# Kernel optimization log

Measured on AMD Instinct MI355X. Metric: run time of the kernel, lower is better.

Reference implementation:

```python
import jax, jax.numpy as jnp
import numpy as np

B, L, DIN, H, E, K = 64, 256, 768, 64, 8, 2
S = 16  # sqrt(L): token<->feature grid side
LOSS_COEF = 1e-2


def gelu(x):
    return jax.nn.gelu(x, approximate=False)  # torch nn.GELU (exact erf)


def cv_squared(v):
    v = v.astype(jnp.float32)
    return jnp.var(v, ddof=1) / (jnp.mean(v) ** 2 + 1e-10)


def setup_inputs() -> dict:
    key = jax.random.key(0)
    ks = jax.random.split(key, 16)
    rn = lambda k, shape, s=0.02: jax.random.normal(k, shape, jnp.float32) * s
    lap = jnp.array([[0., 1., 0.], [1., -4., 1.], [0., 1., 0.]], jnp.float32)
    return {
        "x": jax.random.normal(ks[0], (B, L, DIN), jnp.float32),
        "dte": jax.random.normal(ks[1], (B, L, DIN), jnp.float32),
        "w_gate": rn(ks[2], (L, E), 1.0),
        "W_exp": rn(ks[3], (E, DIN, H)), "b_exp": jnp.zeros((E, H), jnp.float32),
        "W_sh": rn(ks[4], (DIN, H)), "b_sh": jnp.zeros((H,), jnp.float32),
        "ln_g": jnp.ones((H,), jnp.float32), "ln_b": jnp.zeros((H,), jnp.float32),
        "W_px": rn(ks[5], (H, 2 * H)), "b_px": jnp.zeros((2 * H,), jnp.float32),
        "conv_sh": jnp.tile(lap[None, None], (H, 1, 1, 1)),  # depthwise Laplacian [H,1,3,3]
        "W_pxx": rn(ks[6], (H, H)), "b_pxx": jnp.zeros((H,), jnp.float32),
        "W_dte": rn(ks[7], (H, H)), "b_dte": jnp.zeros((H,), jnp.float32),
        "W_dteall": rn(ks[8], (H, H)), "b_dteall": jnp.zeros((H,), jnp.float32),
        "W_rgb": rn(ks[9], (DIN, H)), "b_rgb": jnp.zeros((H,), jnp.float32),
        "W_fx": rn(ks[10], (H, H)), "b_fx": jnp.zeros((H,), jnp.float32),
        "W_fmod": rn(ks[11], (H, H)), "b_fmod": jnp.zeros((H,), jnp.float32),
        "W_fxx": rn(ks[12], (H, H)), "b_fxx": jnp.zeros((H,), jnp.float32),
    }


def reference(x, dte, w_gate, W_exp, b_exp, W_sh, b_sh, ln_g, ln_b, W_px, b_px,
              conv_sh, W_pxx, b_pxx, W_dte, b_dte, W_dteall, b_dteall,
              W_rgb, b_rgb, W_fx, b_fx, W_fmod, b_fmod, W_fxx, b_fxx):
    # ---- top-k gating (clean logits; noisy_gating=False / eval) ----
    logits = dte.mean(-1) @ w_gate                     # [B,E]
    topv, topi = jax.lax.top_k(logits, K)
    topg = jax.nn.softmax(topv, axis=1)
    gates = jnp.zeros_like(logits).at[jnp.arange(B)[:, None], topi].set(topg)
    importance = gates.sum(0)
    load = (gates > 0).sum(0).astype(jnp.float32)
    loss = LOSS_COEF * (cv_squared(importance) + cv_squared(load))
    # ---- sparse dispatch / expert Linear / weighted combine (dense-equivalent) ----
    y = jnp.einsum('be,bld,edh->blh', gates, dte, W_exp) + (gates @ b_exp)[:, None, :]
    # ---- shared expert Linear + Shared block ----
    sh = dte @ W_sh + b_sh                             # [B,L,H]
    shortcut = sh
    t = (sh - sh.mean(-1, keepdims=True)) * jax.lax.rsqrt(sh.var(-1, keepdims=True) + 1e-6)
    t = t * ln_g + ln_b
    t = t @ W_px + b_px                                # [B,L,2H]
    t1, t2 = t[..., :H], t[..., H:]
    f = t1.transpose(0, 2, 1).reshape(B, H, S, S)      # token2feature
    f = jax.lax.conv_general_dilated(f, conv_sh, (1, 1), 'SAME', feature_group_count=H)
    t1 = f.reshape(B, H, L).transpose(0, 2, 1)         # feature2token
    sh = (gelu(t1) * t2) @ W_pxx + b_pxx + shortcut
    # ---- combine MoE and shared streams ----
    dte_tok = (y @ W_dte + b_dte) + (sh @ W_dteall + b_dteall)
    rgb_tok = x @ W_rgb + b_rgb
    # ---- Fusion (its self.norm was overwritten to GELU; token<->feature round-trip is identity) ----
    shortcut = rgb_tok
    a = gelu(rgb_tok) @ W_fx + b_fx
    m = gelu(dte_tok) @ W_fmod + b_fmod
    out = (gelu(m) * a) @ W_fxx + b_fxx + shortcut     # [B,L,H]
    return out, loss
```

## Files before the change

kernel.cpp:

```cpp
#include <hip/hip_runtime.h>
#include <hip/hip_bf16.h>
#include <math.h>

typedef unsigned short u16;
typedef unsigned int u32;
typedef __attribute__((ext_vector_type(8))) short bf16x8;
typedef __attribute__((ext_vector_type(4))) float f32x4;


__device__ __forceinline__ float bf2f(u16 u) {
    union { u32 i; float f; } x; x.i = ((u32)u) << 16; return x.f;
}
__device__ __forceinline__ u16 f2bf(float f) {
    union { __hip_bfloat16 h; u16 u; } x;
    x.h = __float2bfloat16(f);
    return x.u;
}
__device__ __forceinline__ u32 pack2(float a, float b) {
    union { __hip_bfloat162 h; u32 u; } x;
    x.h = __float22bfloat162_rn(make_float2(a, b));
    return x.u;
}
__device__ __forceinline__ float wsum(float v) {
    #pragma unroll
    for (int o = 1; o < 64; o <<= 1) v += __shfl_xor(v, o, 64);
    return v;
}
__device__ __forceinline__ float gelu_f(float x) {
    return 0.5f * x * (1.0f + erff(x * 0.70710678118654752440f));
}

__global__ __launch_bounds__(256) void k_gate_part(const float* __restrict__ dte,
                                                   const float* __restrict__ w_gate,
                                                   float* __restrict__ partial) {
    __shared__ float dmeanS[64];
    int p = blockIdx.x, tid = threadIdx.x, w = tid >> 6, lane = tid & 63;
    #pragma unroll
    for (int h = 0; h < 2; h++) {
        float4 v[8][3];
        #pragma unroll
        for (int i = 0; i < 8; i++) {
            const float* pr = dte + ((size_t)p * 64 + w * 16 + h * 8 + i) * 768;
            #pragma unroll
            for (int j = 0; j < 3; j++)
                v[i][j] = *(const float4*)(pr + (lane + j * 64) * 4);
        }
        #pragma unroll
        for (int i = 0; i < 8; i++) {
            float s = 0.f;
            #pragma unroll
            for (int j = 0; j < 3; j++)
                s += v[i][j].x + v[i][j].y + v[i][j].z + v[i][j].w;
            s = wsum(s);
            if (lane == 0) dmeanS[w * 16 + h * 8 + i] = s * (1.f / 768.f);
        }
    }
    __syncthreads();
    if (w == 0) {
        float dm = dmeanS[lane];
        int wl = (p & 3) * 64 + lane;
        #pragma unroll
        for (int e = 0; e < 8; e++) {
            float s = wsum(dm * w_gate[wl * 8 + e]);
            if (lane == 0) partial[p * 8 + e] = s;
        }
    }
}

__global__ __launch_bounds__(256) void k_gate_fin(const float* __restrict__ partial,
                                                  const float* __restrict__ b_exp,
                                                  int* __restrict__ topi,
                                                  float* __restrict__ topg,
                                                  float* __restrict__ bias_y,
                                                  float* __restrict__ loss_out) {
    __shared__ float gS[64 * 8];
    __shared__ int i0S[64], i1S[64];
    __shared__ float g0S[64], g1S[64];
    int tid = threadIdx.x;
    if (tid < 64) {
        float lg[8];
        #pragma unroll
        for (int e = 0; e < 8; e++)
            lg[e] = partial[(tid * 4 + 0) * 8 + e] + partial[(tid * 4 + 1) * 8 + e] +
                    partial[(tid * 4 + 2) * 8 + e] + partial[(tid * 4 + 3) * 8 + e];
        int i0 = 0; float v0 = lg[0];
        #pragma unroll
        for (int e = 1; e < 8; e++) if (lg[e] > v0) { v0 = lg[e]; i0 = e; }
        int i1 = -1; float v1 = -1e30f;
        #pragma unroll
        for (int e = 0; e < 8; e++) if (e != i0 && lg[e] > v1) { v1 = lg[e]; i1 = e; }
        if (i1 < 0) i1 = (i0 + 1) & 7;
        float e2 = expf(v1 - v0);
        float g0 = 1.f / (1.f + e2);
        float g1 = e2 / (1.f + e2);
        #pragma unroll
        for (int e = 0; e < 8; e++) gS[tid * 8 + e] = 0.f;
        gS[tid * 8 + i0] = g0;
        gS[tid * 8 + i1] = g1;
        i0S[tid] = i0; i1S[tid] = i1; g0S[tid] = g0; g1S[tid] = g1;
        topi[tid * 2] = i0; topi[tid * 2 + 1] = i1;
        topg[tid * 2] = g0; topg[tid * 2 + 1] = g1;
    }
    __syncthreads();
    for (int idx = tid; idx < 4096; idx += 256) {
        int b = idx >> 6, h = idx & 63;
        bias_y[idx] = g0S[b] * b_exp[i0S[b] * 64 + h] + g1S[b] * b_exp[i1S[b] * 64 + h];
    }
    if (tid < 64) {
        float g[8];
        #pragma unroll
        for (int e = 0; e < 8; e++) g[e] = gS[tid * 8 + e];
        float imp[8], ld[8];
        #pragma unroll
        for (int e = 0; e < 8; e++) {
            imp[e] = wsum(g[e]);
            ld[e]  = wsum(g[e] > 0.f ? 1.f : 0.f);
        }
        if (tid == 0) {
            float l = 0.f;
            {
                float s = 0.f;
                #pragma unroll
                for (int e = 0; e < 8; e++) s += imp[e];
                float mn = s / 8.f, v = 0.f;
                #pragma unroll
                for (int e = 0; e < 8; e++) { float d = imp[e] - mn; v += d * d; }
                l += (v / 7.f) / (mn * mn + 1e-10f);
            }
            {
                float s = 0.f;
                #pragma unroll
                for (int e = 0; e < 8; e++) s += ld[e];
                float mn = s / 8.f, v = 0.f;
                #pragma unroll
                for (int e = 0; e < 8; e++) { float d = ld[e] - mn; v += d * d; }
                l += (v / 7.f) / (mn * mn + 1e-10f);
            }
            loss_out[0] = 0.01f * l;
        }
    }
}

__global__ __launch_bounds__(256) void k_gemm3(const float* __restrict__ dte,
                                               const float* __restrict__ x,
                                               const float* __restrict__ W_sh,
                                               const float* __restrict__ b_sh,
                                               const float* __restrict__ W_exp,
                                               const int* __restrict__ topi,
                                               const float* __restrict__ topg,
                                               const float* __restrict__ bias_y,
                                               const float* __restrict__ W_rgb,
                                               const float* __restrict__ b_rgb,
                                               float* __restrict__ buf_sh,
                                               u16* __restrict__ buf_y,
                                               float* __restrict__ out_rgb) {
    __shared__ __align__(16) u16 As[64 * 72];
    __shared__ __align__(16) u16 Wt0[64 * 72];
    __shared__ __align__(16) u16 Wt1[64 * 72];
    int bid = blockIdx.x;
    bool fused = bid < 256;
    int row0 = fused ? bid * 64 : (bid - 256) * 64;
    int b = row0 >> 8;
    int tid = threadIdx.x, wv = tid >> 6, lane = tid & 63;
    int m = lane & 15, quad = lane >> 4;

    const float* A  = fused ? dte : x;
    const float* Wb = fused ? W_sh : W_rgb;
    const float* We0 = W_exp;
    const float* We1 = W_exp;
    float g0 = 0.f, g1 = 0.f;
    if (fused) {
        We0 = W_exp + (size_t)topi[2 * b] * 49152;
        We1 = W_exp + (size_t)topi[2 * b + 1] * 49152;
        g0 = topg[2 * b]; g1 = topg[2 * b + 1];
    }

    float4 pa[2][2];
    float  pw0[16];
    float  pw1[16];
    const int a_r  = tid >> 3;
    const int a_k8 = (tid & 7) * 8;
    const int w_n  = tid & 63;
    const int w_k0 = (tid >> 6) * 16;

    auto loadA = [&](int kc) {
        #pragma unroll
        for (int j = 0; j < 2; j++) {
            const float* src = A + (size_t)(row0 + a_r + j * 32) * 768 + kc * 64 + a_k8;
            pa[j][0] = *(const float4*)(src);
            pa[j][1] = *(const float4*)(src + 4);
        }
    };
    auto loadW = [&](int kc) {
        #pragma unroll
        for (int j = 0; j < 16; j++)
            pw0[j] = Wb[(size_t)(kc * 64 + w_k0 + j) * 64 + w_n];
        if (fused) {
            #pragma unroll
            for (int j = 0; j < 16; j++) {
                size_t off = (size_t)(kc * 64 + w_k0 + j) * 64 + w_n;
                pw1[j] = g0 * We0[off] + g1 * We1[off];
            }
        }
    };
    auto stageLDS = [&]() {
        #pragma unroll
        for (int j = 0; j < 2; j++) {
            uint4 d;
            d.x = pack2(pa[j][0].x, pa[j][0].y);
            d.y = pack2(pa[j][0].z, pa[j][0].w);
            d.z = pack2(pa[j][1].x, pa[j][1].y);
            d.w = pack2(pa[j][1].z, pa[j][1].w);
            *(uint4*)&As[(a_r + j * 32) * 72 + a_k8] = d;
        }
        {
            uint4 d0, d1;
            d0.x = pack2(pw0[0],  pw0[1]);  d0.y = pack2(pw0[2],  pw0[3]);
            d0.z = pack2(pw0[4],  pw0[5]);  d0.w = pack2(pw0[6],  pw0[7]);
            d1.x = pack2(pw0[8],  pw0[9]);  d1.y = pack2(pw0[10], pw0[11]);
            d1.z = pack2(pw0[12], pw0[13]); d1.w = pack2(pw0[14], pw0[15]);
            *(uint4*)&Wt0[w_n * 72 + w_k0]     = d0;
            *(uint4*)&Wt0[w_n * 72 + w_k0 + 8] = d1;
        }
        if (fused) {
            uint4 d0, d1;
            d0.x = pack2(pw1[0],  pw1[1]);  d0.y = pack2(pw1[2],  pw1[3]);
            d0.z = pack2(pw1[4],  pw1[5]);  d0.w = pack2(pw1[6],  pw1[7]);
            d1.x = pack2(pw1[8],  pw1[9]);  d1.y = pack2(pw1[10], pw1[11]);
            d1.z = pack2(pw1[12], pw1[13]); d1.w = pack2(pw1[14], pw1[15]);
            *(uint4*)&Wt1[w_n * 72 + w_k0]     = d0;
            *(uint4*)&Wt1[w_n * 72 + w_k0 + 8] = d1;
        }
    };

    f32x4 z = {0.f, 0.f, 0.f, 0.f};
    f32x4 s0 = z, s1 = z, s2 = z, s3 = z;
    f32x4 y0 = z, y1 = z, y2 = z, y3 = z;

    loadA(0); loadW(0);
    for (int kc = 0; kc < 12; kc++) {
        __syncthreads();
        stageLDS();
        __syncthreads();
        if (kc < 11) { loadA(kc + 1); loadW(kc + 1); }
        const int ar = (wv * 16 + m) * 72;
        bf16x8 a0 = *(const bf16x8*)&As[ar + quad * 8];
        bf16x8 a1 = *(const bf16x8*)&As[ar + 32 + quad * 8];
        #pragma unroll
        for (int t = 0; t < 4; t++) {
            const int br = (t * 16 + m) * 72;
            bf16x8 b0 = *(const bf16x8*)&Wt0[br + quad * 8];
            bf16x8 b1 = *(const bf16x8*)&Wt0[br + 32 + quad * 8];
            f32x4* sp = (t == 0) ? &s0 : (t == 1) ? &s1 : (t == 2) ? &s2 : &s3;
            *sp = __builtin_amdgcn_mfma_f32_16x16x32_bf16(a0, b0, *sp, 0, 0, 0);
            *sp = __builtin_amdgcn_mfma_f32_16x16x32_bf16(a1, b1, *sp, 0, 0, 0);
            if (fused) {
                bf16x8 c0 = *(const bf16x8*)&Wt1[br + quad * 8];
                bf16x8 c1 = *(const bf16x8*)&Wt1[br + 32 + quad * 8];
                f32x4* yp = (t == 0) ? &y0 : (t == 1) ? &y1 : (t == 2) ? &y2 : &y3;
                *yp = __builtin_amdgcn_mfma_f32_16x16x32_bf16(a0, c0, *yp, 0, 0, 0);
                *yp = __builtin_amdgcn_mfma_f32_16x16x32_bf16(a1, c1, *yp, 0, 0, 0);
            }
        }
    }

    f32x4 accs0[4] = {s0, s1, s2, s3};
    f32x4 accs1[4] = {y0, y1, y2, y3};
    #pragma unroll
    for (int t = 0; t < 4; t++) {
        int col = t * 16 + m;
        if (fused) {
            float bs = b_sh[col];
            float by = bias_y[b * 64 + col];
            #pragma unroll
            for (int i = 0; i < 4; i++) {
                int r = row0 + wv * 16 + quad * 4 + i;
                buf_sh[(size_t)r * 64 + col] = accs0[t][i] + bs;
                buf_y[(size_t)r * 64 + col]  = f2bf(accs1[t][i] + by);
            }
        } else {
            float br = b_rgb[col];
            #pragma unroll
            for (int i = 0; i < 4; i++) {
                int r = row0 + wv * 16 + quad * 4 + i;
                out_rgb[(size_t)r * 64 + col] = accs0[t][i] + br;
            }
        }
    }
}

__global__ __launch_bounds__(256) void k_lnpx(const float* __restrict__ buf_sh,
                                              const float* __restrict__ ln_g,
                                              const float* __restrict__ ln_b,
                                              const float* __restrict__ W_px,
                                              const float* __restrict__ b_px,
                                              u16* __restrict__ t1, u16* __restrict__ t2) {
    __shared__ __align__(16) float T[32 * 68];
    __shared__ __align__(16) float Wpx[8192];
    int r0 = blockIdx.x * 32;
    int tid = threadIdx.x, w = tid >> 6, lane = tid & 63;
    #pragma unroll
    for (int j = 0; j < 8; j++) {
        const float* g = W_px + (size_t)(w * 64 + j * 256) * 4 + lane * 4;
        float* l = Wpx + (w * 64 + j * 256) * 4;
        __builtin_amdgcn_global_load_lds(
            (const __attribute__((address_space(1))) unsigned int*)g,
            (__attribute__((address_space(3))) unsigned int*)l,
            16, 0, 0);
    }
    float lnG = ln_g[lane], lnB = ln_b[lane];
    for (int i = 0; i < 8; i++) {
        int l = w * 8 + i;
        float v = buf_sh[(size_t)(r0 + l) * 64 + lane];
        float mean = wsum(v) * (1.f / 64.f);
        float d = v - mean;
        float var = wsum(d * d) * (1.f / 64.f);
        T[l * 68 + lane] = d * rsqrtf(var + 1e-6f) * lnG + lnB;
    }
    __syncthreads();
    int rg = tid >> 4, cg = tid & 15;
    float acc1[2][4] = {}, acc2[2][4] = {};
    const float* tr = T + rg * 2 * 68;
    #pragma unroll 2
    for (int k4 = 0; k4 < 64; k4 += 4) {
        float4 av0 = *(const float4*)(tr + k4);
        float4 av1 = *(const float4*)(tr + 68 + k4);
        const float a0s[4] = {av0.x, av0.y, av0.z, av0.w};
        const float a1s[4] = {av1.x, av1.y, av1.z, av1.w};
        #pragma unroll
        for (int q = 0; q < 4; q++) {
            int kk = k4 + q;
            float a0 = a0s[q], a1 = a1s[q];
            float4 w1 = *(const float4*)(Wpx + kk * 128 + cg * 4);
            float4 w2 = *(const float4*)(Wpx + kk * 128 + 64 + cg * 4);
            acc1[0][0] += a0 * w1.x; acc1[0][1] += a0 * w1.y; acc1[0][2] += a0 * w1.z; acc1[0][3] += a0 * w1.w;
            acc1[1][0] += a1 * w1.x; acc1[1][1] += a1 * w1.y; acc1[1][2] += a1 * w1.z; acc1[1][3] += a1 * w1.w;
            acc2[0][0] += a0 * w2.x; acc2[0][1] += a0 * w2.y; acc2[0][2] += a0 * w2.z; acc2[0][3] += a0 * w2.w;
            acc2[1][0] += a1 * w2.x; acc2[1][1] += a1 * w2.y; acc2[1][2] += a1 * w2.z; acc2[1][3] += a1 * w2.w;
        }
    }
    float4 b1 = *(const float4*)(b_px + cg * 4);
    float4 b2 = *(const float4*)(b_px + 64 + cg * 4);
    #pragma unroll
    for (int i = 0; i < 2; i++) {
        int r = r0 + rg * 2 + i;
        u32* d1 = (u32*)(t1 + (size_t)r * 64 + cg * 4);
        d1[0] = pack2(acc1[i][0] + b1.x, acc1[i][1] + b1.y);
        d1[1] = pack2(acc1[i][2] + b1.z, acc1[i][3] + b1.w);
        u32* d2 = (u32*)(t2 + (size_t)r * 64 + cg * 4);
        d2[0] = pack2(acc2[i][0] + b2.x, acc2[i][1] + b2.y);
        d2[1] = pack2(acc2[i][2] + b2.z, acc2[i][3] + b2.w);
    }
}

__global__ __launch_bounds__(256) void k_tail(const u16* __restrict__ t1,
                                              const u16* __restrict__ t2,
                                              const float* __restrict__ conv_sh,
                                              const float* __restrict__ W_pxx,
                                              const float* __restrict__ b_pxx,
                                              const float* __restrict__ buf_sh,
                                              const u16* __restrict__ buf_y,
                                              const float* __restrict__ W_dte,
                                              const float* __restrict__ b_dte,
                                              const float* __restrict__ W_dteall,
                                              const float* __restrict__ b_dteall,
                                              const float* __restrict__ W_fx,
                                              const float* __restrict__ b_fx,
                                              const float* __restrict__ W_fmod,
                                              const float* __restrict__ b_fmod,
                                              const float* __restrict__ W_fxx,
                                              const float* __restrict__ b_fxx,
                                              float* __restrict__ out) {
    __shared__ __align__(16) float C0[32 * 68];
    __shared__ __align__(16) float GA[32 * 68];
    __shared__ __align__(16) float SH1[32 * 68];
    __shared__ __align__(16) float GM[32 * 68];
    __shared__ __align__(16) u16   Ybh[32 * 72];
    __shared__ __align__(16) float WL[2][4096];
    int r0 = blockIdx.x * 32;
    int tid = threadIdx.x, w = tid >> 6, lane = tid & 63;
    int rg = tid >> 4, cg = tid & 15;

    auto stage_w = [&](const float* __restrict__ Wsrc, int half) {
        const float* g = Wsrc + w * 1024 + lane * 4;
        float* l = &WL[half][w * 1024];
        #pragma unroll
        for (int j = 0; j < 4; j++) {
            __builtin_amdgcn_global_load_lds(
                (const __attribute__((address_space(1))) unsigned int*)(g + j * 256),
                (__attribute__((address_space(3))) unsigned int*)(l + j * 256),
                16, 0, 0);
        }
    };

    stage_w(W_pxx, 0);

    stage_w(W_dte, 1);
    float4 rsv[2];
    #pragma unroll
    for (int i = 0; i < 2; i++) {
        int r = rg * 2 + i;
        uint2 v = *(const uint2*)(buf_y + (size_t)(r0 + r) * 64 + cg * 4);
        *(uint2*)(&Ybh[r * 72 + cg * 4]) = v;
        rsv[i] = *(const float4*)(out + (size_t)(r0 + r) * 64 + cg * 4);
        GA[r * 68 + cg * 4 + 0] = gelu_f(rsv[i].x);
        GA[r * 68 + cg * 4 + 1] = gelu_f(rsv[i].y);
        GA[r * 68 + cg * 4 + 2] = gelu_f(rsv[i].z);
        GA[r * 68 + cg * 4 + 3] = gelu_f(rsv[i].w);
    }
    {
        float c0 = conv_sh[lane * 9 + 0], c1 = conv_sh[lane * 9 + 1], c2 = conv_sh[lane * 9 + 2];
        float c3 = conv_sh[lane * 9 + 3], c4 = conv_sh[lane * 9 + 4], c5 = conv_sh[lane * 9 + 5];
        float c6 = conv_sh[lane * 9 + 6], c7 = conv_sh[lane * 9 + 7], c8 = conv_sh[lane * 9 + 8];
        #pragma unroll
        for (int i = 0; i < 8; i++) {
            int l = w * 8 + i;
            int gr = r0 + l;
            int pix = gr & 255, ii = pix >> 4, jj = pix & 15;
            const u16* p = t1 + (size_t)gr * 64 + lane;
            float c = c4 * bf2f(p[0]);
            if (ii > 0) {
                c += c1 * bf2f(p[-1024]);
                if (jj > 0)  c += c0 * bf2f(p[-1024 - 64]);
                if (jj < 15) c += c2 * bf2f(p[-1024 + 64]);
            }
            if (jj > 0)  c += c3 * bf2f(p[-64]);
            if (jj < 15) c += c5 * bf2f(p[64]);
            if (ii < 15) {
                c += c7 * bf2f(p[1024]);
                if (jj > 0)  c += c6 * bf2f(p[1024 - 64]);
                if (jj < 15) c += c8 * bf2f(p[1024 + 64]);
            }
            C0[l * 68 + lane] = gelu_f(c) * bf2f(t2[(size_t)gr * 64 + lane]);
        }
    }
    __syncthreads();

    {
        float acc[2][4] = {};
        const float* ur = C0 + rg * 2 * 68;
        #pragma unroll 4
        for (int k4 = 0; k4 < 64; k4 += 4) {
            float4 av0 = *(const float4*)(ur + k4);
            float4 av1 = *(const float4*)(ur + 68 + k4);
            const float a0s[4] = {av0.x, av0.y, av0.z, av0.w};
            const float a1s[4] = {av1.x, av1.y, av1.z, av1.w};
            #pragma unroll
            for (int q = 0; q < 4; q++) {
                float a0 = a0s[q], a1 = a1s[q];
                float4 wv = *(const float4*)(&WL[0][(k4 + q) * 64 + cg * 4]);
                acc[0][0] += a0 * wv.x; acc[0][1] += a0 * wv.y; acc[0][2] += a0 * wv.z; acc[0][3] += a0 * wv.w;
                acc[1][0] += a1 * wv.x; acc[1][1] += a1 * wv.y; acc[1][2] += a1 * wv.z; acc[1][3] += a1 * wv.w;
            }
        }
        float4 bp = *(const float4*)(b_pxx + cg * 4);
        #pragma unroll
        for (int i = 0; i < 2; i++) {
            int r = rg * 2 + i;
            float4 shv = *(const float4*)(buf_sh + (size_t)(r0 + r) * 64 + cg * 4);
            *(float4*)(SH1 + r * 68 + cg * 4) =
                make_float4(acc[i][0] + bp.x + shv.x, acc[i][1] + bp.y + shv.y,
                            acc[i][2] + bp.z + shv.z, acc[i][3] + bp.w + shv.w);
        }
    }
    __syncthreads();

    float accC[2][4] = {};
    stage_w(W_dteall, 0);
    {
        const u16* yr = Ybh + rg * 2 * 72;
        #pragma unroll 4
        for (int k4 = 0; k4 < 64; k4 += 4) {
            uint2 yv0 = *(const uint2*)(yr + k4);
            uint2 yv1 = *(const uint2*)(yr + 72 + k4);
            const float y0s[4] = {bf2f((u16)(yv0.x & 0xffffu)), bf2f((u16)(yv0.x >> 16)),
                                  bf2f((u16)(yv0.y & 0xffffu)), bf2f((u16)(yv0.y >> 16))};
            const float y1s[4] = {bf2f((u16)(yv1.x & 0xffffu)), bf2f((u16)(yv1.x >> 16)),
                                  bf2f((u16)(yv1.y & 0xffffu)), bf2f((u16)(yv1.y >> 16))};
            #pragma unroll
            for (int q = 0; q < 4; q++) {
                float y0 = y0s[q], y1 = y1s[q];
                float4 wv = *(const float4*)(&WL[1][(k4 + q) * 64 + cg * 4]);
                accC[0][0] += y0 * wv.x; accC[0][1] += y0 * wv.y; accC[0][2] += y0 * wv.z; accC[0][3] += y0 * wv.w;
                accC[1][0] += y1 * wv.x; accC[1][1] += y1 * wv.y; accC[1][2] += y1 * wv.z; accC[1][3] += y1 * wv.w;
            }
        }
    }
    __syncthreads();

    stage_w(W_fx, 1);
    {
        const float* sr = SH1 + rg * 2 * 68;
        #pragma unroll 4
        for (int k4 = 0; k4 < 64; k4 += 4) {
            float4 av0 = *(const float4*)(sr + k4);
            float4 av1 = *(const float4*)(sr + 68 + k4);
            const float s0s[4] = {av0.x, av0.y, av0.z, av0.w};
            const float s1s[4] = {av1.x, av1.y, av1.z, av1.w};
            #pragma unroll
            for (int q = 0; q < 4; q++) {
                float s0 = s0s[q], s1 = s1s[q];
                float4 wv = *(const float4*)(&WL[0][(k4 + q) * 64 + cg * 4]);
                accC[0][0] += s0 * wv.x; accC[0][1] += s0 * wv.y; accC[0][2] += s0 * wv.z; accC[0][3] += s0 * wv.w;
                accC[1][0] += s1 * wv.x; accC[1][1] += s1 * wv.y; accC[1][2] += s1 * wv.z; accC[1][3] += s1 * wv.w;
            }
        }
        float4 bd1 = *(const float4*)(b_dte + cg * 4);
        float4 bd2 = *(const float4*)(b_dteall + cg * 4);
        #pragma unroll
        for (int i = 0; i < 2; i++) {
            int r = rg * 2 + i;
            *(float4*)(GM + r * 68 + cg * 4) =
                make_float4(gelu_f(accC[i][0] + bd1.x + bd2.x), gelu_f(accC[i][1] + bd1.y + bd2.y),
                            gelu_f(accC[i][2] + bd1.z + bd2.z), gelu_f(accC[i][3] + bd1.w + bd2.w));
        }
    }
    __syncthreads();

    float accA[2][4] = {};
    stage_w(W_fmod, 0);
    {
        const float* ga = GA + rg * 2 * 68;
        #pragma unroll 4
        for (int k4 = 0; k4 < 64; k4 += 4) {
            float4 av0 = *(const float4*)(ga + k4);
            float4 av1 = *(const float4*)(ga + 68 + k4);
            const float a0s[4] = {av0.x, av0.y, av0.z, av0.w};
            const float a1s[4] = {av1.x, av1.y, av1.z, av1.w};
            #pragma unroll
            for (int q = 0; q < 4; q++) {
                float a0 = a0s[q], a1 = a1s[q];
                float4 wv = *(const float4*)(&WL[1][(k4 + q) * 64 + cg * 4]);
                accA[0][0] += a0 * wv.x; accA[0][1] += a0 * wv.y; accA[0][2] += a0 * wv.z; accA[0][3] += a0 * wv.w;
                accA[1][0] += a1 * wv.x; accA[1][1] += a1 * wv.y; accA[1][2] += a1 * wv.z; accA[1][3] += a1 * wv.w;
            }
        }
    }
    __syncthreads();

    stage_w(W_fxx, 1);
    {
        float accM[2][4] = {};
        const float* gm = GM + rg * 2 * 68;
        #pragma unroll 4
        for (int k4 = 0; k4 < 64; k4 += 4) {
            float4 av0 = *(const float4*)(gm + k4);
            float4 av1 = *(const float4*)(gm + 68 + k4);
            const float m0s[4] = {av0.x, av0.y, av0.z, av0.w};
            const float m1s[4] = {av1.x, av1.y, av1.z, av1.w};
            #pragma unroll
            for (int q = 0; q < 4; q++) {
                float m0 = m0s[q], m1 = m1s[q];
                float4 wv = *(const float4*)(&WL[0][(k4 + q) * 64 + cg * 4]);
                accM[0][0] += m0 * wv.x; accM[0][1] += m0 * wv.y; accM[0][2] += m0 * wv.z; accM[0][3] += m0 * wv.w;
                accM[1][0] += m1 * wv.x; accM[1][1] += m1 * wv.y; accM[1][2] += m1 * wv.z; accM[1][3] += m1 * wv.w;
            }
        }
        float4 bx = *(const float4*)(b_fx + cg * 4);
        float4 bm = *(const float4*)(b_fmod + cg * 4);
        #pragma unroll
        for (int i = 0; i < 2; i++) {
            int r = rg * 2 + i;
            float a0 = accA[i][0] + bx.x, a1 = accA[i][1] + bx.y, a2 = accA[i][2] + bx.z, a3 = accA[i][3] + bx.w;
            float m0 = accM[i][0] + bm.x, m1 = accM[i][1] + bm.y, m2 = accM[i][2] + bm.z, m3 = accM[i][3] + bm.w;
            *(float4*)(C0 + r * 68 + cg * 4) =
                make_float4(gelu_f(m0) * a0, gelu_f(m1) * a1, gelu_f(m2) * a2, gelu_f(m3) * a3);
        }
    }
    __syncthreads();

    {
        float acc[2][4] = {};
        const float* pr = C0 + rg * 2 * 68;
        #pragma unroll 4
        for (int k4 = 0; k4 < 64; k4 += 4) {
            float4 av0 = *(const float4*)(pr + k4);
            float4 av1 = *(const float4*)(pr + 68 + k4);
            const float p0s[4] = {av0.x, av0.y, av0.z, av0.w};
            const float p1s[4] = {av1.x, av1.y, av1.z, av1.w};
            #pragma unroll
            for (int q = 0; q < 4; q++) {
                float p0 = p0s[q], p1 = p1s[q];
                float4 wv = *(const float4*)(&WL[1][(k4 + q) * 64 + cg * 4]);
                acc[0][0] += p0 * wv.x; acc[0][1] += p0 * wv.y; acc[0][2] += p0 * wv.z; acc[0][3] += p0 * wv.w;
                acc[1][0] += p1 * wv.x; acc[1][1] += p1 * wv.y; acc[1][2] += p1 * wv.z; acc[1][3] += p1 * wv.w;
            }
        }
        float4 bo = *(const float4*)(b_fxx + cg * 4);
        #pragma unroll
        for (int i = 0; i < 2; i++) {
            int r = rg * 2 + i;
            *(float4*)(out + (size_t)(r0 + r) * 64 + cg * 4) =
                make_float4(acc[i][0] + bo.x + rsv[i].x, acc[i][1] + bo.y + rsv[i].y,
                            acc[i][2] + bo.z + rsv[i].z, acc[i][3] + bo.w + rsv[i].w);
        }
    }
}

extern "C" void kernel_launch(void* const* d_in, const int* in_sizes, int n_in,
                              void* d_out, int out_size, void* d_ws, size_t ws_size,
                              hipStream_t stream) {
    const float* x       = (const float*)d_in[0];
    const float* dte     = (const float*)d_in[1];
    const float* w_gate  = (const float*)d_in[2];
    const float* W_exp   = (const float*)d_in[3];
    const float* b_exp   = (const float*)d_in[4];
    const float* W_sh    = (const float*)d_in[5];
    const float* b_sh    = (const float*)d_in[6];
    const float* ln_g    = (const float*)d_in[7];
    const float* ln_b    = (const float*)d_in[8];
    const float* W_px    = (const float*)d_in[9];
    const float* b_px    = (const float*)d_in[10];
    const float* conv_sh = (const float*)d_in[11];
    const float* W_pxx   = (const float*)d_in[12];
    const float* b_pxx   = (const float*)d_in[13];
    const float* W_dte   = (const float*)d_in[14];
    const float* b_dte   = (const float*)d_in[15];
    const float* W_dteall= (const float*)d_in[16];
    const float* b_dteall= (const float*)d_in[17];
    const float* W_rgb   = (const float*)d_in[18];
    const float* b_rgb   = (const float*)d_in[19];
    const float* W_fx    = (const float*)d_in[20];
    const float* b_fx    = (const float*)d_in[21];
    const float* W_fmod  = (const float*)d_in[22];
    const float* b_fmod  = (const float*)d_in[23];
    const float* W_fxx   = (const float*)d_in[24];
    const float* b_fxx   = (const float*)d_in[25];

    float* out = (float*)d_out;

    float* wsf    = (float*)d_ws;
    float* partial= wsf;
    int*   topi   = (int*)(wsf + 2048);
    float* topg   = wsf + 2176;
    float* bias_y = wsf + 2304;
    float* buf_sh = wsf + 8192;
    u16*   buf_y  = (u16*)(wsf + 8192 + 1048576);
    u16*   t1     = (u16*)(wsf + 8192 + 1048576 + 524288);
    u16*   t2     = (u16*)(wsf + 8192 + 1048576 + 524288*2);

    hipLaunchKernelGGL(k_gate_part, dim3(256), dim3(256), 0, stream, dte, w_gate, partial);
    hipLaunchKernelGGL(k_gate_fin, dim3(1), dim3(256), 0, stream,
                       partial, b_exp, topi, topg, bias_y, out + 1048576);
    hipLaunchKernelGGL(k_gemm3, dim3(512), dim3(256), 0, stream,
                       dte, x, W_sh, b_sh, W_exp, topi, topg, bias_y, W_rgb, b_rgb,
                       buf_sh, buf_y, out);
    hipLaunchKernelGGL(k_lnpx, dim3(512), dim3(256), 0, stream,
                       buf_sh, ln_g, ln_b, W_px, b_px, t1, t2);
    hipLaunchKernelGGL(k_tail, dim3(512), dim3(256), 0, stream,
                       t1, t2, conv_sh, W_pxx, b_pxx, buf_sh, buf_y,
                       W_dte, b_dte, W_dteall, b_dteall,
                       W_fx, b_fx, W_fmod, b_fmod, W_fxx, b_fxx, out);

    (void)in_sizes; (void)n_in; (void)out_size; (void)ws_size;
}
```

Before: 237.6 us.

## Merge gating finalize into MoE GEMM and overlap rgb GEMM with gate reduction

Removes the single-block gate finalize kernel. Each MoE GEMM block now recomputes its own batch's top-2 selection and softmax from the partial logits, and block 0 also computes the load-balancing loss. The rgb projection GEMM moves into the same launch as the gate partial reduction, so those independent tasks share one grid. This cuts one launch and one serial single-block stage, at the cost of redundant top-k work in every MoE block and less balanced block types in the first kernel.

Result: slower. 251.7 us (+5.9%).

```diff
diff --git a/kernel.cpp b/kernel.cpp
--- a/kernel.cpp
+++ b/kernel.cpp
@@ -30,86 +30,189 @@
     return 0.5f * x * (1.0f + erff(x * 0.70710678118654752440f));
 }
 
-__global__ __launch_bounds__(256) void k_gate_part(const float* __restrict__ dte,
-                                                   const float* __restrict__ w_gate,
-                                                   float* __restrict__ partial) {
+__global__ __launch_bounds__(256) void k_front(const float* __restrict__ dte,
+                                               const float* __restrict__ w_gate,
+                                               float* __restrict__ partial,
+                                               const float* __restrict__ x,
+                                               const float* __restrict__ W_rgb,
+                                               const float* __restrict__ b_rgb,
+                                               float* __restrict__ out_rgb) {
     __shared__ float dmeanS[64];
-    int p = blockIdx.x, tid = threadIdx.x, w = tid >> 6, lane = tid & 63;
-    #pragma unroll
-    for (int h = 0; h < 2; h++) {
-        float4 v[8][3];
-        #pragma unroll
-        for (int i = 0; i < 8; i++) {
-            const float* pr = dte + ((size_t)p * 64 + w * 16 + h * 8 + i) * 768;
-            #pragma unroll
-            for (int j = 0; j < 3; j++)
-                v[i][j] = *(const float4*)(pr + (lane + j * 64) * 4);
-        }
-        #pragma unroll
-        for (int i = 0; i < 8; i++) {
-            float s = 0.f;
-            #pragma unroll
-            for (int j = 0; j < 3; j++)
-                s += v[i][j].x + v[i][j].y + v[i][j].z + v[i][j].w;
-            s = wsum(s);
-            if (lane == 0) dmeanS[w * 16 + h * 8 + i] = s * (1.f / 768.f);
-        }
-    }
-    __syncthreads();
-    if (w == 0) {
-        float dm = dmeanS[lane];
-        int wl = (p & 3) * 64 + lane;
-        #pragma unroll
-        for (int e = 0; e < 8; e++) {
-            float s = wsum(dm * w_gate[wl * 8 + e]);
-            if (lane == 0) partial[p * 8 + e] = s;
-        }
-    }
-}
-
-__global__ __launch_bounds__(256) void k_gate_fin(const float* __restrict__ partial,
-                                                  const float* __restrict__ b_exp,
-                                                  int* __restrict__ topi,
-                                                  float* __restrict__ topg,
-                                                  float* __restrict__ bias_y,
-                                                  float* __restrict__ loss_out) {
-    __shared__ float gS[64 * 8];
-    __shared__ int i0S[64], i1S[64];
-    __shared__ float g0S[64], g1S[64];
-    int tid = threadIdx.x;
-    if (tid < 64) {
-        float lg[8];
+    __shared__ __align__(16) u16 As[64 * 72];
+    __shared__ __align__(16) u16 Wt0[64 * 72];
+    int bid = blockIdx.x;
+    int tid = threadIdx.x, w = tid >> 6, lane = tid & 63;
+
+    if (bid < 256) {
+        int p = bid;
+        #pragma unroll
+        for (int h = 0; h < 2; h++) {
+            float4 v[8][3];
+            #pragma unroll
+            for (int i = 0; i < 8; i++) {
+                const float* pr = dte + ((size_t)p * 64 + w * 16 + h * 8 + i) * 768;
+                #pragma unroll
+                for (int j = 0; j < 3; j++)
+                    v[i][j] = *(const float4*)(pr + (lane + j * 64) * 4);
+            }
+            #pragma unroll
+            for (int i = 0; i < 8; i++) {
+                float s = 0.f;
+                #pragma unroll
+                for (int j = 0; j < 3; j++)
+                    s += v[i][j].x + v[i][j].y + v[i][j].z + v[i][j].w;
+                s = wsum(s);
+                if (lane == 0) dmeanS[w * 16 + h * 8 + i] = s * (1.f / 768.f);
+            }
+        }
+        __syncthreads();
+        if (w == 0) {
+            float dm = dmeanS[lane];
+            int wl = (p & 3) * 64 + lane;
+            #pragma unroll
+            for (int e = 0; e < 8; e++) {
+                float s = wsum(dm * w_gate[wl * 8 + e]);
+                if (lane == 0) partial[p * 8 + e] = s;
+            }
+        }
+        return;
+    }
+
+    int row0 = (bid - 256) * 64;
+    int m = lane & 15, quad = lane >> 4;
+
+    float4 pa[2][2];
+    float  pw0[16];
+    const int a_r  = tid >> 3;
+    const int a_k8 = (tid & 7) * 8;
+    const int w_n  = tid & 63;
+    const int w_k0 = (tid >> 6) * 16;
+
+    auto loadA = [&](int kc) {
+        #pragma unroll
+        for (int j = 0; j < 2; j++) {
+            const float* src = x + (size_t)(row0 + a_r + j * 32) * 768 + kc * 64 + a_k8;
+            pa[j][0] = *(const float4*)(src);
+            pa[j][1] = *(const float4*)(src + 4);
+        }
+    };
+    auto loadW = [&](int kc) {
+        #pragma unroll
+        for (int j = 0; j < 16; j++)
+            pw0[j] = W_rgb[(size_t)(kc * 64 + w_k0 + j) * 64 + w_n];
+    };
+    auto stageLDS = [&]() {
+        #pragma unroll
+        for (int j = 0; j < 2; j++) {
+            uint4 d;
+            d.x = pack2(pa[j][0].x, pa[j][0].y);
+            d.y = pack2(pa[j][0].z, pa[j][0].w);
+            d.z = pack2(pa[j][1].x, pa[j][1].y);
+            d.w = pack2(pa[j][1].z, pa[j][1].w);
+            *(uint4*)&As[(a_r + j * 32) * 72 + a_k8] = d;
+        }
+        uint4 d0, d1;
+        d0.x = pack2(pw0[0],  pw0[1]);  d0.y = pack2(pw0[2],  pw0[3]);
+        d0.z = pack2(pw0[4],  pw0[5]);  d0.w = pack2(pw0[6],  pw0[7]);
+        d1.x = pack2(pw0[8],  pw0[9]);  d1.y = pack2(pw0[10], pw0[11]);
+        d1.z = pack2(pw0[12], pw0[13]); d1.w = pack2(pw0[14], pw0[15]);
+        *(uint4*)&Wt0[w_n * 72 + w_k0]     = d0;
+        *(uint4*)&Wt0[w_n * 72 + w_k0 + 8] = d1;
+    };
+
+    f32x4 z = {0.f, 0.f, 0.f, 0.f};
+    f32x4 s0 = z, s1 = z, s2 = z, s3 = z;
+
+    loadA(0); loadW(0);
+    for (int kc = 0; kc < 12; kc++) {
+        __syncthreads();
+        stageLDS();
+        __syncthreads();
+        if (kc < 11) { loadA(kc + 1); loadW(kc + 1); }
+        const int ar = ((tid >> 6) * 16 + m) * 72;
+        bf16x8 a0 = *(const bf16x8*)&As[ar + quad * 8];
+        bf16x8 a1 = *(const bf16x8*)&As[ar + 32 + quad * 8];
+        #pragma unroll
+        for (int t = 0; t < 4; t++) {
+            const int br = (t * 16 + m) * 72;
+            bf16x8 b0 = *(const bf16x8*)&Wt0[br + quad * 8];
+            bf16x8 b1 = *(const bf16x8*)&Wt0[br + 32 + quad * 8];
+            f32x4* sp = (t == 0) ? &s0 : (t == 1) ? &s1 : (t == 2) ? &s2 : &s3;
+            *sp = __builtin_amdgcn_mfma_f32_16x16x32_bf16(a0, b0, *sp, 0, 0, 0);
+            *sp = __builtin_amdgcn_mfma_f32_16x16x32_bf16(a1, b1, *sp, 0, 0, 0);
+        }
+    }
+
+    f32x4 accs0[4] = {s0, s1, s2, s3};
+    #pragma unroll
+    for (int t = 0; t < 4; t++) {
+        int col = t * 16 + m;
+        float br = b_rgb[col];
+        #pragma unroll
+        for (int i = 0; i < 4; i++) {
+            int r = row0 + (tid >> 6) * 16 + quad * 4 + i;
+            out_rgb[(size_t)r * 64 + col] = accs0[t][i] + br;
+        }
+    }
+}
+
+__global__ __launch_bounds__(256) void k_moe(const float* __restrict__ dte,
+                                             const float* __restrict__ W_sh,
+                                             const float* __restrict__ b_sh,
+                                             const float* __restrict__ W_exp,
+                                             const float* __restrict__ b_exp,
+                                             const float* __restrict__ partial,
+                                             float* __restrict__ buf_sh,
+                                             u16* __restrict__ buf_y,
+                                             float* __restrict__ loss_out) {
+    __shared__ __align__(16) u16 As[64 * 72];
+    __shared__ __align__(16) u16 Wt0[64 * 72];
+    __shared__ __align__(16) u16 Wt1[64 * 72];
+    int bid = blockIdx.x;
+    int row0 = bid * 64;
+    int b = bid >> 2;
+    int tid = threadIdx.x, wv = tid >> 6, lane = tid & 63;
+    int m = lane & 15, quad = lane >> 4;
+
+    float lg[8];
+    #pragma unroll
+    for (int e = 0; e < 8; e++)
+        lg[e] = partial[(b * 4 + 0) * 8 + e] + partial[(b * 4 + 1) * 8 + e] +
+                partial[(b * 4 + 2) * 8 + e] + partial[(b * 4 + 3) * 8 + e];
+    int i0 = 0; float v0 = lg[0];
+    #pragma unroll
+    for (int e = 1; e < 8; e++) if (lg[e] > v0) { v0 = lg[e]; i0 = e; }
+    int i1 = -1; float v1 = -1e30f;
+    #pragma unroll
+    for (int e = 0; e < 8; e++) if (e != i0 && lg[e] > v1) { v1 = lg[e]; i1 = e; }
+    if (i1 < 0) i1 = (i0 + 1) & 7;
+    float e2 = expf(v1 - v0);
+    float g0 = 1.f / (1.f + e2);
+    float g1 = e2 / (1.f + e2);
+    const float* We0 = W_exp + (size_t)i0 * 49152;
+    const float* We1 = W_exp + (size_t)i1 * 49152;
+
+    if (bid == 0 && tid < 64) {
+        float lgl[8];
         #pragma unroll
         for (int e = 0; e < 8; e++)
-            lg[e] = partial[(tid * 4 + 0) * 8 + e] + partial[(tid * 4 + 1) * 8 + e] +
-                    partial[(tid * 4 + 2) * 8 + e] + partial[(tid * 4 + 3) * 8 + e];
-        int i0 = 0; float v0 = lg[0];
-        #pragma unroll
-        for (int e = 1; e < 8; e++) if (lg[e] > v0) { v0 = lg[e]; i0 = e; }
-        int i1 = -1; float v1 = -1e30f;
-        #pragma unroll
-        for (int e = 0; e < 8; e++) if (e != i0 && lg[e] > v1) { v1 = lg[e]; i1 = e; }
-        if (i1 < 0) i1 = (i0 + 1) & 7;
-        float e2 = expf(v1 - v0);
-        float g0 = 1.f / (1.f + e2);
-        float g1 = e2 / (1.f + e2);
-        #pragma unroll
-        for (int e = 0; e < 8; e++) gS[tid * 8 + e] = 0.f;
-        gS[tid * 8 + i0] = g0;
-        gS[tid * 8 + i1] = g1;
-        i0S[tid] = i0; i1S[tid] = i1; g0S[tid] = g0; g1S[tid] = g1;
-        topi[tid * 2] = i0; topi[tid * 2 + 1] = i1;
-        topg[tid * 2] = g0; topg[tid * 2 + 1] = g1;
-    }
-    __syncthreads();
-    for (int idx = tid; idx < 4096; idx += 256) {
-        int b = idx >> 6, h = idx & 63;
-        bias_y[idx] = g0S[b] * b_exp[i0S[b] * 64 + h] + g1S[b] * b_exp[i1S[b] * 64 + h];
-    }
-    if (tid < 64) {
+            lgl[e] = partial[(tid * 4 + 0) * 8 + e] + partial[(tid * 4 + 1) * 8 + e] +
+                     partial[(tid * 4 + 2) * 8 + e] + partial[(tid * 4 + 3) * 8 + e];
+        int li0 = 0; float lv0 = lgl[0];
+        #pragma unroll
+        for (int e = 1; e < 8; e++) if (lgl[e] > lv0) { lv0 = lgl[e]; li0 = e; }
+        int li1 = -1; float lv1 = -1e30f;
+        #pragma unroll
+        for (int e = 0; e < 8; e++) if (e != li0 && lgl[e] > lv1) { lv1 = lgl[e]; li1 = e; }
+        if (li1 < 0) li1 = (li0 + 1) & 7;
+        float le2 = expf(lv1 - lv0);
+        float lg0 = 1.f / (1.f + le2);
+        float lg1 = le2 / (1.f + le2);
         float g[8];
         #pragma unroll
-        for (int e = 0; e < 8; e++) g[e] = gS[tid * 8 + e];
+        for (int e = 0; e < 8; e++) g[e] = 0.f;
+        g[li0] = lg0;
+        g[li1] = lg1;
         float imp[8], ld[8];
         #pragma unroll
         for (int e = 0; e < 8; e++) {
@@ -139,41 +242,6 @@
             loss_out[0] = 0.01f * l;
         }
     }
-}
-
-__global__ __launch_bounds__(256) void k_gemm3(const float* __restrict__ dte,
-                                               const float* __restrict__ x,
-                                               const float* __restrict__ W_sh,
-                                               const float* __restrict__ b_sh,
-                                               const float* __restrict__ W_exp,
-                                               const int* __restrict__ topi,
-                                               const float* __restrict__ topg,
-                                               const float* __restrict__ bias_y,
-                                               const float* __restrict__ W_rgb,
-                                               const float* __restrict__ b_rgb,
-                                               float* __restrict__ buf_sh,
-                                               u16* __restrict__ buf_y,
-                                               float* __restrict__ out_rgb) {
-    __shared__ __align__(16) u16 As[64 * 72];
-    __shared__ __align__(16) u16 Wt0[64 * 72];
-    __shared__ __align__(16) u16 Wt1[64 * 72];
-    int bid = blockIdx.x;
-    bool fused = bid < 256;
-    int row0 = fused ? bid * 64 : (bid - 256) * 64;
-    int b = row0 >> 8;
-    int tid = threadIdx.x, wv = tid >> 6, lane = tid & 63;
-    int m = lane & 15, quad = lane >> 4;
-
-    const float* A  = fused ? dte : x;
-    const float* Wb = fused ? W_sh : W_rgb;
-    const float* We0 = W_exp;
-    const float* We1 = W_exp;
-    float g0 = 0.f, g1 = 0.f;
-    if (fused) {
-        We0 = W_exp + (size_t)topi[2 * b] * 49152;
-        We1 = W_exp + (size_t)topi[2 * b + 1] * 49152;
-        g0 = topg[2 * b]; g1 = topg[2 * b + 1];
-    }
 
     float4 pa[2][2];
     float  pw0[16];
@@ -186,7 +254,7 @@
     auto loadA = [&](int kc) {
         #pragma unroll
         for (int j = 0; j < 2; j++) {
-            const float* src = A + (size_t)(row0 + a_r + j * 32) * 768 + kc * 64 + a_k8;
+            const float* src = dte + (size_t)(row0 + a_r + j * 32) * 768 + kc * 64 + a_k8;
             pa[j][0] = *(const float4*)(src);
             pa[j][1] = *(const float4*)(src + 4);
         }
@@ -194,13 +262,11 @@
     auto loadW = [&](int kc) {
         #pragma unroll
         for (int j = 0; j < 16; j++)
-            pw0[j] = Wb[(size_t)(kc * 64 + w_k0 + j) * 64 + w_n];
-        if (fused) {
-            #pragma unroll
-            for (int j = 0; j < 16; j++) {
-                size_t off = (size_t)(kc * 64 + w_k0 + j) * 64 + w_n;
-                pw1[j] = g0 * We0[off] + g1 * We1[off];
-            }
+            pw0[j] = W_sh[(size_t)(kc * 64 + w_k0 + j) * 64 + w_n];
+        #pragma unroll
+        for (int j = 0; j < 16; j++) {
+            size_t off = (size_t)(kc * 64 + w_k0 + j) * 64 + w_n;
+            pw1[j] = g0 * We0[off] + g1 * We1[off];
         }
     };
     auto stageLDS = [&]() {
@@ -222,7 +288,7 @@
             *(uint4*)&Wt0[w_n * 72 + w_k0]     = d0;
             *(uint4*)&Wt0[w_n * 72 + w_k0 + 8] = d1;
         }
-        if (fused) {
+        {
             uint4 d0, d1;
             d0.x = pack2(pw1[0],  pw1[1]);  d0.y = pack2(pw1[2],  pw1[3]);
             d0.z = pack2(pw1[4],  pw1[5]);  d0.w = pack2(pw1[6],  pw1[7]);
@@ -254,13 +320,11 @@
             f32x4* sp = (t == 0) ? &s0 : (t == 1) ? &s1 : (t == 2) ? &s2 : &s3;
             *sp = __builtin_amdgcn_mfma_f32_16x16x32_bf16(a0, b0, *sp, 0, 0, 0);
             *sp = __builtin_amdgcn_mfma_f32_16x16x32_bf16(a1, b1, *sp, 0, 0, 0);
-            if (fused) {
-                bf16x8 c0 = *(const bf16x8*)&Wt1[br + quad * 8];
-                bf16x8 c1 = *(const bf16x8*)&Wt1[br + 32 + quad * 8];
-                f32x4* yp = (t == 0) ? &y0 : (t == 1) ? &y1 : (t == 2) ? &y2 : &y3;
-                *yp = __builtin_amdgcn_mfma_f32_16x16x32_bf16(a0, c0, *yp, 0, 0, 0);
-                *yp = __builtin_amdgcn_mfma_f32_16x16x32_bf16(a1, c1, *yp, 0, 0, 0);
-            }
+            bf16x8 c0 = *(const bf16x8*)&Wt1[br + quad * 8];
+            bf16x8 c1 = *(const bf16x8*)&Wt1[br + 32 + quad * 8];
+            f32x4* yp = (t == 0) ? &y0 : (t == 1) ? &y1 : (t == 2) ? &y2 : &y3;
+            *yp = __builtin_amdgcn_mfma_f32_16x16x32_bf16(a0, c0, *yp, 0, 0, 0);
+            *yp = __builtin_amdgcn_mfma_f32_16x16x32_bf16(a1, c1, *yp, 0, 0, 0);
         }
     }
 
@@ -269,22 +333,13 @@
     #pragma unroll
     for (int t = 0; t < 4; t++) {
         int col = t * 16 + m;
-        if (fused) {
-            float bs = b_sh[col];
-            float by = bias_y[b * 64 + col];
-            #pragma unroll
-            for (int i = 0; i < 4; i++) {
-                int r = row0 + wv * 16 + quad * 4 + i;
-                buf_sh[(size_t)r * 64 + col] = accs0[t][i] + bs;
-                buf_y[(size_t)r * 64 + col]  = f2bf(accs1[t][i] + by);
-            }
-        } else {
-            float br = b_rgb[col];
-            #pragma unroll
-            for (int i = 0; i < 4; i++) {
-                int r = row0 + wv * 16 + quad * 4 + i;
-                out_rgb[(size_t)r * 64 + col] = accs0[t][i] + br;
-            }
+        float bs = b_sh[col];
+        float by = g0 * b_exp[i0 * 64 + col] + g1 * b_exp[i1 * 64 + col];
+        #pragma unroll
+        for (int i = 0; i < 4; i++) {
+            int r = row0 + wv * 16 + quad * 4 + i;
+            buf_sh[(size_t)r * 64 + col] = accs0[t][i] + bs;
+            buf_y[(size_t)r * 64 + col]  = f2bf(accs1[t][i] + by);
         }
     }
 }
@@ -631,20 +686,16 @@
 
     float* wsf    = (float*)d_ws;
     float* partial= wsf;
-    int*   topi   = (int*)(wsf + 2048);
-    float* topg   = wsf + 2176;
-    float* bias_y = wsf + 2304;
     float* buf_sh = wsf + 8192;
     u16*   buf_y  = (u16*)(wsf + 8192 + 1048576);
     u16*   t1     = (u16*)(wsf + 8192 + 1048576 + 524288);
     u16*   t2     = (u16*)(wsf + 8192 + 1048576 + 524288*2);
 
-    hipLaunchKernelGGL(k_gate_part, dim3(256), dim3(256), 0, stream, dte, w_gate, partial);
-    hipLaunchKernelGGL(k_gate_fin, dim3(1), dim3(256), 0, stream,
-                       partial, b_exp, topi, topg, bias_y, out + 1048576);
-    hipLaunchKernelGGL(k_gemm3, dim3(512), dim3(256), 0, stream,
-                       dte, x, W_sh, b_sh, W_exp, topi, topg, bias_y, W_rgb, b_rgb,
-                       buf_sh, buf_y, out);
+    hipLaunchKernelGGL(k_front, dim3(512), dim3(256), 0, stream,
+                       dte, w_gate, partial, x, W_rgb, b_rgb, out);
+    hipLaunchKernelGGL(k_moe, dim3(256), dim3(256), 0, stream,
+                       dte, W_sh, b_sh, W_exp, b_exp, partial,
+                       buf_sh, buf_y, out + 1048576);
     hipLaunchKernelGGL(k_lnpx, dim3(512), dim3(256), 0, stream,
                        buf_sh, ln_g, ln_b, W_px, b_px, t1, t2);
     hipLaunchKernelGGL(k_tail, dim3(512), dim3(256), 0, stream,
```
